# Kernel optimization log

Measured on AMD Instinct MI355X. Metric: run time of the kernel, lower is better.

Reference implementation:

```python
import jax, jax.numpy as jnp
import numpy as np
from jax import lax

HEADS = 16
HEAD_DIM = 64
EPS = 1e-5

def _act_quant(x):
    # per-token int8 absmax quantization (BitNet b1.58)
    scale = 127.0 / jnp.clip(jnp.max(jnp.abs(x), axis=-1, keepdims=True), EPS)
    return jnp.clip(jnp.round(x * scale), -128.0, 127.0) / scale

def _weight_quant(w):
    # ternary weight quantization with mean-absmax scale
    scale = 1.0 / jnp.clip(jnp.mean(jnp.abs(w)), EPS)
    return jnp.clip(jnp.round(w * scale), -1.0, 1.0) / scale

def bitlinear(x, w):
    # straight-through estimator: forward uses quantized, backward sees identity
    xq = x + lax.stop_gradient(_act_quant(x) - x)
    wq = w + lax.stop_gradient(_weight_quant(w) - w)
    return jnp.einsum('bsd,od->bso', xq, wq)

def setup_inputs() -> dict:
    key = jax.random.key(0)
    ks = jax.random.split(key, 5)
    B, S, D = 2, 2048, 1024
    x = jax.random.normal(ks[0], (B, S, D), dtype=jnp.float32)
    # causal mask (B, 1, S, S): 1 = keep, 0 = masked
    mask = jnp.broadcast_to(jnp.tril(jnp.ones((S, S), dtype=jnp.int32))[None, None], (B, 1, S, S))
    scale = 0.02
    Wq = jax.random.normal(ks[1], (D, D), dtype=jnp.float32) * scale
    Wk = jax.random.normal(ks[2], (D, D), dtype=jnp.float32) * scale
    Wv = jax.random.normal(ks[3], (D, D), dtype=jnp.float32) * scale
    Wo = jax.random.normal(ks[4], (D, D), dtype=jnp.float32) * scale
    return {"x": x, "mask": mask, "Wq": Wq, "Wk": Wk, "Wv": Wv, "Wo": Wo}

def reference(x, mask, Wq, Wk, Wv, Wo):
    B, S, D = x.shape
    H, Hd = HEADS, HEAD_DIM
    q = bitlinear(x, Wq).reshape(B, S, H, Hd).transpose(0, 2, 1, 3)  # (B,H,S,Hd)
    k = bitlinear(x, Wk).reshape(B, S, H, Hd).transpose(0, 2, 1, 3)
    v = bitlinear(x, Wv).reshape(B, S, H, Hd).transpose(0, 2, 1, 3)
    attn = jnp.einsum('bhsd,bhtd->bhst', q, k) / jnp.sqrt(jnp.float32(Hd))
    attn = jnp.where(mask == 0, -jnp.inf, attn)
    attn = jax.nn.softmax(attn, axis=-1)
    out = jnp.einsum('bhst,bhtd->bhsd', attn, v)
    out = out.transpose(0, 2, 1, 3).reshape(B, S, D)
    return bitlinear(out, Wo)
```

## Files before the change

### kernel.cpp

```cpp
#include <hip/hip_runtime.h>
#include <hip/hip_bf16.h>
#include <math.h>


typedef float  f32x4  __attribute__((ext_vector_type(4)));
typedef __bf16 bf16x8 __attribute__((ext_vector_type(8)));
typedef __bf16 bf16x4 __attribute__((ext_vector_type(4)));
typedef unsigned int u32x4 __attribute__((ext_vector_type(4)));

#define EPSV 1e-5f

__device__ __forceinline__ f32x4 mfma16(bf16x8 a, bf16x8 b, f32x4 c) {
    return __builtin_amdgcn_mfma_f32_16x16x32_bf16(a, b, c, 0, 0, 0);
}

__device__ __forceinline__ void gload16(const void* g, void* lds) {
    __builtin_amdgcn_global_load_lds((const __attribute__((address_space(1))) unsigned int*)g,
                                     (__attribute__((address_space(3))) unsigned int*)lds, 16, 0, 0);
}

__global__ __launch_bounds__(256) void k_wsum(const float* __restrict__ w0, const float* __restrict__ w1,
                                              const float* __restrict__ w2, const float* __restrict__ w3,
                                              double* __restrict__ wsum) {
    int w = blockIdx.x >> 6, chunk = blockIdx.x & 63, tid = threadIdx.x;
    const float* W = (w == 0) ? w0 : (w == 1) ? w1 : (w == 2) ? w2 : w3;
    const float* base = W + (size_t)chunk * 16384;
    float s = 0.f;
#pragma unroll
    for (int i = 0; i < 16; i++) {
        f32x4 v = *(const f32x4*)(base + i * 1024 + tid * 4);
        s += fabsf(v.x) + fabsf(v.y) + fabsf(v.z) + fabsf(v.w);
    }
#pragma unroll
    for (int off = 1; off < 64; off <<= 1) s += __shfl_xor(s, off);
    __shared__ float red[4];
    if ((tid & 63) == 0) red[tid >> 6] = s;
    __syncthreads();
    if (tid == 0) {
        double t = (double)red[0] + (double)red[1] + (double)red[2] + (double)red[3];
        atomicAdd(&wsum[w], t);
    }
}

__global__ __launch_bounds__(256) void k_wquant(const float* __restrict__ w0, const float* __restrict__ w1,
                                                const float* __restrict__ w2, const float* __restrict__ w3,
                                                const double* __restrict__ wsum,
                                                __bf16* __restrict__ wq, float* __restrict__ wm) {
    int w = blockIdx.y;
    const float* W = (w == 0) ? w0 : (w == 1) ? w1 : (w == 2) ? w2 : w3;
    float mean = (float)(wsum[w] * (1.0 / 1048576.0));
    float ms = fmaxf(mean, EPSV);
    float scale = 1.0f / ms;
    int pos = blockIdx.x * 1024 + threadIdx.x * 4;
    f32x4 v = *(const f32x4*)(W + pos);
    float q0 = fminf(fmaxf(rintf(v.x * scale), -1.f), 1.f);
    float q1 = fminf(fmaxf(rintf(v.y * scale), -1.f), 1.f);
    float q2 = fminf(fmaxf(rintf(v.z * scale), -1.f), 1.f);
    float q3 = fminf(fmaxf(rintf(v.w * scale), -1.f), 1.f);
    unsigned int b0 = __builtin_bit_cast(unsigned short, (__bf16)q0);
    unsigned int b1 = __builtin_bit_cast(unsigned short, (__bf16)q1);
    unsigned int b2 = __builtin_bit_cast(unsigned short, (__bf16)q2);
    unsigned int b3 = __builtin_bit_cast(unsigned short, (__bf16)q3);
    uint2 p; p.x = b0 | (b1 << 16); p.y = b2 | (b3 << 16);
    *(uint2*)(wq + (size_t)w * 1048576 + pos) = p;
    if (blockIdx.x == 0 && threadIdx.x == 0) wm[w] = ms;
}

__global__ __launch_bounds__(256) void k_actq(const float* __restrict__ in, __bf16* __restrict__ outq,
                                              float* __restrict__ rs) {
    int t = blockIdx.x, tid = threadIdx.x;
    const float* row = in + (size_t)t * 1024;
    f32x4 v = *(const f32x4*)(row + tid * 4);
    float am = fmaxf(fmaxf(fabsf(v.x), fabsf(v.y)), fmaxf(fabsf(v.z), fabsf(v.w)));
#pragma unroll
    for (int off = 1; off < 64; off <<= 1) am = fmaxf(am, __shfl_xor(am, off));
    __shared__ float red[4];
    if ((tid & 63) == 0) red[tid >> 6] = am;
    __syncthreads();
    am = fmaxf(fmaxf(red[0], red[1]), fmaxf(red[2], red[3]));
    am = fmaxf(am, EPSV);
    float scale = 127.0f / am;
    float q0 = fminf(fmaxf(rintf(v.x * scale), -128.f), 127.f);
    float q1 = fminf(fmaxf(rintf(v.y * scale), -128.f), 127.f);
    float q2 = fminf(fmaxf(rintf(v.z * scale), -128.f), 127.f);
    float q3 = fminf(fmaxf(rintf(v.w * scale), -128.f), 127.f);
    unsigned int b0 = __builtin_bit_cast(unsigned short, (__bf16)q0);
    unsigned int b1 = __builtin_bit_cast(unsigned short, (__bf16)q1);
    unsigned int b2 = __builtin_bit_cast(unsigned short, (__bf16)q2);
    unsigned int b3 = __builtin_bit_cast(unsigned short, (__bf16)q3);
    uint2 p; p.x = b0 | (b1 << 16); p.y = b2 | (b3 << 16);
    *(uint2*)(outq + (size_t)t * 1024 + tid * 4) = p;
    if (tid == 0) rs[t] = am / 127.0f;
}

template <int MODE>
__global__ __launch_bounds__(256) void k_gemm(const __bf16* __restrict__ X, const __bf16* __restrict__ Wb,
                                              const float* __restrict__ rs, const float* __restrict__ wm,
                                              __bf16* __restrict__ o0, __bf16* __restrict__ o1,
                                              __bf16* __restrict__ o2, float* __restrict__ outf) {
    __shared__ __attribute__((aligned(16))) __bf16 As[128 * 32];
    __shared__ __attribute__((aligned(16))) __bf16 Bs[128 * 32];
    int tid = threadIdx.x;
    int wave = tid >> 6, lane = tid & 63, g = lane >> 4, l = lane & 15;
    int m0 = blockIdx.x * 128, n0 = blockIdx.y * 128;
    int z = blockIdx.z;
    const __bf16* W = Wb + (size_t)z * 1048576;
    float wmv = wm[z];
    f32x4 acc[4][4] = {};
    int srow0 = wave * 16 + (lane >> 2);
    int scol = (lane & 3) * 8;
    const __bf16* Ag = X + (size_t)(m0 + srow0) * 1024 + scol;
    const __bf16* Bg = W + (size_t)(n0 + srow0) * 1024 + scol;
    __bf16* ldsA = As + wave * 512;
    __bf16* ldsB = Bs + wave * 512;
    int wrow = (wave >> 1) * 64, wcol = (wave & 1) * 64;
    bool vswap = (MODE == 0) && (z == 2);
    for (int k0 = 0; k0 < 1024; k0 += 32) {
        __syncthreads();
        gload16(Ag + k0,             ldsA);
        gload16(Ag + 64 * 1024 + k0, ldsA + 2048);
        gload16(Bg + k0,             ldsB);
        gload16(Bg + 64 * 1024 + k0, ldsB + 2048);
        __syncthreads();
        bf16x8 af[4], bfr[4];
#pragma unroll
        for (int i = 0; i < 4; i++) af[i]  = *(const bf16x8*)&As[(wrow + i * 16 + l) * 32 + 8 * g];
#pragma unroll
        for (int i = 0; i < 4; i++) bfr[i] = *(const bf16x8*)&Bs[(wcol + i * 16 + l) * 32 + 8 * g];
        if (vswap) {
#pragma unroll
            for (int mi = 0; mi < 4; mi++)
#pragma unroll
                for (int ni = 0; ni < 4; ni++)
                    acc[mi][ni] = mfma16(bfr[ni], af[mi], acc[mi][ni]);
        } else {
#pragma unroll
            for (int mi = 0; mi < 4; mi++)
#pragma unroll
                for (int ni = 0; ni < 4; ni++)
                    acc[mi][ni] = mfma16(af[mi], bfr[ni], acc[mi][ni]);
        }
    }
    if (vswap) {
#pragma unroll
        for (int mi = 0; mi < 4; mi++) {
            int m = m0 + wrow + mi * 16 + l;
            float rsm = rs[m] * wmv;
            int b = m >> 11, s2 = m & 2047;
#pragma unroll
            for (int ni = 0; ni < 4; ni++) {
                int nb = n0 + wcol + ni * 16 + 4 * g;
#pragma unroll
                for (int r = 0; r < 4; r++) {
                    int n = nb + r;
                    int h = n >> 6, hd = n & 63;
                    o2[((size_t)(b * 16 + h) * 64 + hd) * 2048 + s2] = (__bf16)(acc[mi][ni][r] * rsm);
                }
            }
        }
        return;
    }
#pragma unroll
    for (int mi = 0; mi < 4; mi++) {
        int mbase = m0 + wrow + mi * 16 + 4 * g;
        f32x4 rv = {rs[mbase], rs[mbase + 1], rs[mbase + 2], rs[mbase + 3]};
#pragma unroll
        for (int ni = 0; ni < 4; ni++) {
            int n = n0 + wcol + ni * 16 + l;
#pragma unroll
            for (int r = 0; r < 4; r++) {
                float v = acc[mi][ni][r] * (rv[r] * wmv);
                if constexpr (MODE == 0) {
                    int m = mbase + r;
                    int b = m >> 11, s2 = m & 2047;
                    int h = n >> 6, hd = n & 63;
                    __bf16* dst = (z == 0) ? o0 : o1;
                    dst[(((size_t)(b * 16 + h)) * 2048 + s2) * 64 + hd] = (__bf16)v;
                } else {
                    outf[(size_t)(mbase + r) * 1024 + n] = v;
                }
            }
        }
    }
}

__global__ __launch_bounds__(512) void k_attn(const __bf16* __restrict__ qg, const __bf16* __restrict__ kb,
                                              const __bf16* __restrict__ vt, float* __restrict__ attn) {
    __shared__ __attribute__((aligned(16))) __bf16 Ks[3][4096];
    __shared__ __attribute__((aligned(16))) __bf16 Vs[3][4096];
    int tid = threadIdx.x, w = tid >> 6, lane = tid & 63, g = lane >> 4, l = lane & 15;
    int bh = blockIdx.y, bq = bh >> 4, h = bh & 15;
    int q0 = blockIdx.x * 128;
    size_t bhq = (size_t)bh * 2048 * 64;
    int qlo = q0 + w * 16, qmax = qlo + 15;
    int qrow = qlo + l;
    bf16x8 aq0 = *(const bf16x8*)(qg + bhq + (size_t)qrow * 64 + 8 * g);
    bf16x8 aq1 = *(const bf16x8*)(qg + bhq + (size_t)qrow * 64 + 32 + 8 * g);
    asm volatile("" : "+v"(aq0), "+v"(aq1));
    f32x4 o[4] = {};
    float mreg = -INFINITY, lsum = 0.f;
    int sRow = w * 8 + (lane >> 3);
    int sCol = ((lane & 7) ^ (lane >> 3)) << 3;
    const __bf16* Kg = kb + bhq + (size_t)sRow * 64 + sCol;
    const __bf16* Vg = vt + bhq + (size_t)sRow * 2048 + sCol;
    int nt = 2 * (blockIdx.x + 1);
    gload16(Kg,        &Ks[0][w * 512]);
    gload16(Vg,        &Vs[0][w * 512]);
    gload16(Kg + 4096, &Ks[1][w * 512]);
    gload16(Vg + 64,   &Vs[1][w * 512]);
    int cur = 0;
    int swk = (l & 7) << 4;
    for (int t = 0; t < nt; ++t) {
        if (t < nt - 1) { asm volatile("s_waitcnt vmcnt(2)"); }
        else            { asm volatile("s_waitcnt vmcnt(0)"); }
        __builtin_amdgcn_s_barrier();
        __builtin_amdgcn_sched_barrier(0);
        int tn = t + 2;
        if (tn < nt) {
            int nbuf = cur + 2; if (nbuf >= 3) nbuf -= 3;
            gload16(Kg + (size_t)tn * 4096, &Ks[nbuf][w * 512]);
            gload16(Vg + tn * 64,           &Vs[nbuf][w * 512]);
        }
        int t0 = t * 64;
        if (t0 <= qmax) {
            const char* Kb = (const char*)&Ks[cur][0];
            const char* Vb = (const char*)&Vs[cur][0];
            f32x4 sv[4];
            __builtin_amdgcn_s_setprio(1);
#pragma unroll
            for (int nb = 0; nb < 4; nb++) {
                const char* kbase = Kb + (nb * 16 + l) * 128;
                bf16x8 bk0 = *(const bf16x8*)(kbase + ((16 * g) ^ swk));
                bf16x8 bk1 = *(const bf16x8*)(kbase + ((64 + 16 * g) ^ swk));
                f32x4 a = {};
                a = mfma16(bk0, aq0, a);
                a = mfma16(bk1, aq1, a);
                sv[nb] = a * 0.125f;
            }
            __builtin_amdgcn_s_setprio(0);
            if (t0 + 63 > qlo) {
#pragma unroll
                for (int nb = 0; nb < 4; nb++)
#pragma unroll
                    for (int r = 0; r < 4; r++) {
                        int key = t0 + nb * 16 + 4 * g + r;
                        if (key > qrow) sv[nb][r] = -INFINITY;
                    }
            }
            float pm0 = fmaxf(fmaxf(sv[0][0], sv[0][1]), fmaxf(sv[0][2], sv[0][3]));
            float pm1 = fmaxf(fmaxf(sv[1][0], sv[1][1]), fmaxf(sv[1][2], sv[1][3]));
            float pm2 = fmaxf(fmaxf(sv[2][0], sv[2][1]), fmaxf(sv[2][2], sv[2][3]));
            float pm3 = fmaxf(fmaxf(sv[3][0], sv[3][1]), fmaxf(sv[3][2], sv[3][3]));
            float pm = fmaxf(fmaxf(pm0, pm1), fmaxf(pm2, pm3));
            pm = fmaxf(pm, __shfl_xor(pm, 16));
            pm = fmaxf(pm, __shfl_xor(pm, 32));
            float mnew = fmaxf(mreg, pm);
            float corr = __expf(mreg - mnew);
            mreg = mnew;
            float psum = 0.f;
#pragma unroll
            for (int nb = 0; nb < 4; nb++)
#pragma unroll
                for (int r = 0; r < 4; r++) {
                    float pe = __expf(sv[nb][r] - mnew);
                    sv[nb][r] = pe;
                    psum += pe;
                }
            psum += __shfl_xor(psum, 16);
            psum += __shfl_xor(psum, 32);
            lsum = lsum * corr + psum;
#pragma unroll
            for (int hb = 0; hb < 4; hb++) o[hb] *= corr;
            bf16x8 pf0, pf1;
#pragma unroll
            for (int j = 0; j < 8; j++) {
                pf0[j] = (__bf16)sv[j >> 2][j & 3];
                pf1[j] = (__bf16)sv[2 + (j >> 2)][j & 3];
            }
            __builtin_amdgcn_s_setprio(1);
#pragma unroll
            for (int hb = 0; hb < 4; hb++) {
                int vrow = hb * 16 + l;
                const char* vb = Vb + vrow * 128;
                int rsw = vrow & 7;
                int ib = 8 * (g & 1);
                int gh = g >> 1;
                bf16x4 v00 = *(const bf16x4*)(vb + 16 * ((gh + 0) ^ rsw) + ib);
                bf16x4 v01 = *(const bf16x4*)(vb + 16 * ((gh + 2) ^ rsw) + ib);
                bf16x8 vf0 = __builtin_shufflevector(v00, v01, 0, 1, 2, 3, 4, 5, 6, 7);
                o[hb] = mfma16(vf0, pf0, o[hb]);
                bf16x4 v10 = *(const bf16x4*)(vb + 16 * ((gh + 4) ^ rsw) + ib);
                bf16x4 v11 = *(const bf16x4*)(vb + 16 * ((gh + 6) ^ rsw) + ib);
                bf16x8 vf1 = __builtin_shufflevector(v10, v11, 0, 1, 2, 3, 4, 5, 6, 7);
                o[hb] = mfma16(vf1, pf1, o[hb]);
            }
            __builtin_amdgcn_s_setprio(0);
        }
        cur = (cur + 1 == 3) ? 0 : cur + 1;
    }
    float inv = 1.0f / lsum;
    float* dst = attn + ((size_t)(bq * 2048 + qlo + l)) * 1024 + h * 64 + 4 * g;
#pragma unroll
    for (int hb = 0; hb < 4; hb++) {
        f32x4 vsto = o[hb] * inv;
        *(f32x4*)(dst + 16 * hb) = vsto;
    }
}

extern "C" void kernel_launch(void* const* d_in, const int* in_sizes, int n_in,
                              void* d_out, int out_size, void* d_ws, size_t ws_size,
                              hipStream_t stream) {
    const float* x  = (const float*)d_in[0];
    const float* Wq = (const float*)d_in[2];
    const float* Wk = (const float*)d_in[3];
    const float* Wv = (const float*)d_in[4];
    const float* Wo = (const float*)d_in[5];
    float* out = (float*)d_out;
    char* ws = (char*)d_ws;

    double* wsumd = (double*)(ws + 0);
    float*  wmv   = (float*)(ws + 256);
    __bf16* wqall = (__bf16*)(ws + 512);
    __bf16* xq    = (__bf16*)(ws + 512 + 8388608);
    float*  rsx   = (float*)(ws + 512 + 16777216);
    float*  rso   = (float*)(ws + 512 + 16777216 + 16384);
    char*   big   = ws + 512 + 16777216 + 32768;
    __bf16* qbuf  = (__bf16*)(big);
    __bf16* kbuf  = (__bf16*)(big + 8388608);
    __bf16* oq    = (__bf16*)(big + 16777216);
    __bf16* vtb   = (__bf16*)(big + 25165824);
    float*  attn  = (float*)(big + 33554432);

    hipMemsetAsync(ws, 0, 512, stream);
    k_wsum<<<dim3(256), 256, 0, stream>>>(Wq, Wk, Wv, Wo, wsumd);
    k_wquant<<<dim3(1024, 4), 256, 0, stream>>>(Wq, Wk, Wv, Wo, wsumd, wqall, wmv);
    k_actq<<<dim3(4096), 256, 0, stream>>>(x, xq, rsx);
    k_gemm<0><<<dim3(32, 8, 3), 256, 0, stream>>>(xq, wqall, rsx, wmv, qbuf, kbuf, vtb, nullptr);
    k_attn<<<dim3(16, 32), 512, 0, stream>>>(qbuf, kbuf, vtb, attn);
    k_actq<<<dim3(4096), 256, 0, stream>>>(attn, oq, rso);
    k_gemm<1><<<dim3(32, 8, 1), 256, 0, stream>>>(oq, wqall + 3 * 1048576, rso, wmv + 3,
                                                  nullptr, nullptr, nullptr, out);
}
```

Measured before the change: 254.1 us.

## Double-buffer GEMM LDS tiles and balance causal attention block scheduling

The GEMM kernel now uses two LDS buffers, prefetching the next K-slice while computing on the current one, with a single barrier per iteration instead of two. The attention kernel remaps query tile indices so blocks with long and short causal ranges are interleaved across the grid for better load balance. Drawbacks: LDS use doubles, and the barrier's implicit vmcnt wait may still serialise part of the prefetch.

```diff
diff --git a/kernel.cpp b/kernel.cpp
--- a/kernel.cpp
+++ b/kernel.cpp
@@ -98,8 +98,8 @@
                                               const float* __restrict__ rs, const float* __restrict__ wm,
                                               __bf16* __restrict__ o0, __bf16* __restrict__ o1,
                                               __bf16* __restrict__ o2, float* __restrict__ outf) {
-    __shared__ __attribute__((aligned(16))) __bf16 As[128 * 32];
-    __shared__ __attribute__((aligned(16))) __bf16 Bs[128 * 32];
+    __shared__ __attribute__((aligned(16))) __bf16 As[2][4096];
+    __shared__ __attribute__((aligned(16))) __bf16 Bs[2][4096];
     int tid = threadIdx.x;
     int wave = tid >> 6, lane = tid & 63, g = lane >> 4, l = lane & 15;
     int m0 = blockIdx.x * 128, n0 = blockIdx.y * 128;
@@ -111,22 +111,28 @@
     int scol = (lane & 3) * 8;
     const __bf16* Ag = X + (size_t)(m0 + srow0) * 1024 + scol;
     const __bf16* Bg = W + (size_t)(n0 + srow0) * 1024 + scol;
-    __bf16* ldsA = As + wave * 512;
-    __bf16* ldsB = Bs + wave * 512;
+    int woff = wave * 512;
     int wrow = (wave >> 1) * 64, wcol = (wave & 1) * 64;
     bool vswap = (MODE == 0) && (z == 2);
+    gload16(Ag,             &As[0][woff]);
+    gload16(Ag + 64 * 1024, &As[0][woff + 2048]);
+    gload16(Bg,             &Bs[0][woff]);
+    gload16(Bg + 64 * 1024, &Bs[0][woff + 2048]);
+    __syncthreads();
     for (int k0 = 0; k0 < 1024; k0 += 32) {
-        __syncthreads();
-        gload16(Ag + k0,             ldsA);
-        gload16(Ag + 64 * 1024 + k0, ldsA + 2048);
-        gload16(Bg + k0,             ldsB);
-        gload16(Bg + 64 * 1024 + k0, ldsB + 2048);
-        __syncthreads();
+        int cur = (k0 >> 5) & 1;
+        if (k0 + 32 < 1024) {
+            int nxt = cur ^ 1;
+            gload16(Ag + k0 + 32,             &As[nxt][woff]);
+            gload16(Ag + 64 * 1024 + k0 + 32, &As[nxt][woff + 2048]);
+            gload16(Bg + k0 + 32,             &Bs[nxt][woff]);
+            gload16(Bg + 64 * 1024 + k0 + 32, &Bs[nxt][woff + 2048]);
+        }
         bf16x8 af[4], bfr[4];
 #pragma unroll
-        for (int i = 0; i < 4; i++) af[i]  = *(const bf16x8*)&As[(wrow + i * 16 + l) * 32 + 8 * g];
-#pragma unroll
-        for (int i = 0; i < 4; i++) bfr[i] = *(const bf16x8*)&Bs[(wcol + i * 16 + l) * 32 + 8 * g];
+        for (int i = 0; i < 4; i++) af[i]  = *(const bf16x8*)&As[cur][(wrow + i * 16 + l) * 32 + 8 * g];
+#pragma unroll
+        for (int i = 0; i < 4; i++) bfr[i] = *(const bf16x8*)&Bs[cur][(wcol + i * 16 + l) * 32 + 8 * g];
         if (vswap) {
 #pragma unroll
             for (int mi = 0; mi < 4; mi++)
@@ -140,6 +146,7 @@
                 for (int ni = 0; ni < 4; ni++)
                     acc[mi][ni] = mfma16(af[mi], bfr[ni], acc[mi][ni]);
         }
+        __syncthreads();
     }
     if (vswap) {
 #pragma unroll
@@ -190,7 +197,9 @@
     __shared__ __attribute__((aligned(16))) __bf16 Vs[3][4096];
     int tid = threadIdx.x, w = tid >> 6, lane = tid & 63, g = lane >> 4, l = lane & 15;
     int bh = blockIdx.y, bq = bh >> 4, h = bh & 15;
-    int q0 = blockIdx.x * 128;
+    int xt = (blockIdx.x + blockIdx.y) & 15;
+    int xs = (blockIdx.y & 16) ? (15 - xt) : xt;
+    int q0 = xs * 128;
     size_t bhq = (size_t)bh * 2048 * 64;
     int qlo = q0 + w * 16, qmax = qlo + 15;
     int qrow = qlo + l;
@@ -203,7 +212,7 @@
     int sCol = ((lane & 7) ^ (lane >> 3)) << 3;
     const __bf16* Kg = kb + bhq + (size_t)sRow * 64 + sCol;
     const __bf16* Vg = vt + bhq + (size_t)sRow * 2048 + sCol;
-    int nt = 2 * (blockIdx.x + 1);
+    int nt = 2 * (xs + 1);
     gload16(Kg,        &Ks[0][w * 512]);
     gload16(Vg,        &Vs[0][w * 512]);
     gload16(Kg + 4096, &Ks[1][w * 512]);
```

Result: faster. 242.9 us (-4.4%).

## Double-buffer GEMM LDS tiles with swizzle and rebalance causal attention block order

Applied to the files above, without the earlier changes.

The GEMM moves from a single-buffered 32-wide K tile to a double-buffered 64-wide K tile. It uses an XOR-swizzled LDS layout and raises wave priority around the MFMA bursts, so global-to-LDS loads overlap compute, there are fewer barriers, and bank conflicts drop. The attention kernel remaps block indices so heavy and light causal query tiles interleave in launch order, which should give better load balance across CUs. In exchange, the GEMM uses more LDS, which may lower occupancy, and the index math gets more complex.

```diff
diff --git a/kernel.cpp b/kernel.cpp
--- a/kernel.cpp
+++ b/kernel.cpp
@@ -98,8 +98,8 @@
                                               const float* __restrict__ rs, const float* __restrict__ wm,
                                               __bf16* __restrict__ o0, __bf16* __restrict__ o1,
                                               __bf16* __restrict__ o2, float* __restrict__ outf) {
-    __shared__ __attribute__((aligned(16))) __bf16 As[128 * 32];
-    __shared__ __attribute__((aligned(16))) __bf16 Bs[128 * 32];
+    __shared__ __attribute__((aligned(16))) __bf16 As[2][8192];
+    __shared__ __attribute__((aligned(16))) __bf16 Bs[2][8192];
     int tid = threadIdx.x;
     int wave = tid >> 6, lane = tid & 63, g = lane >> 4, l = lane & 15;
     int m0 = blockIdx.x * 128, n0 = blockIdx.y * 128;
@@ -107,39 +107,60 @@
     const __bf16* W = Wb + (size_t)z * 1048576;
     float wmv = wm[z];
     f32x4 acc[4][4] = {};
-    int srow0 = wave * 16 + (lane >> 2);
-    int scol = (lane & 3) * 8;
-    const __bf16* Ag = X + (size_t)(m0 + srow0) * 1024 + scol;
-    const __bf16* Bg = W + (size_t)(n0 + srow0) * 1024 + scol;
-    __bf16* ldsA = As + wave * 512;
-    __bf16* ldsB = Bs + wave * 512;
+    int sRow = wave * 32 + (lane >> 3);
+    int sCol = 8 * ((lane & 7) ^ (lane >> 3));
+    const __bf16* Ag = X + (size_t)(m0 + sRow) * 1024 + sCol;
+    const __bf16* Bg = W + (size_t)(n0 + sRow) * 1024 + sCol;
     int wrow = (wave >> 1) * 64, wcol = (wave & 1) * 64;
     bool vswap = (MODE == 0) && (z == 2);
-    for (int k0 = 0; k0 < 1024; k0 += 32) {
+#pragma unroll
+    for (int j = 0; j < 4; j++) {
+        gload16(Ag + (size_t)j * 8192, &As[0][(wave * 4 + j) * 512]);
+        gload16(Bg + (size_t)j * 8192, &Bs[0][(wave * 4 + j) * 512]);
+    }
+    __syncthreads();
+    for (int t = 0; t < 16; ++t) {
+        int cur = t & 1;
+        if (t < 15) {
+            int nxt = cur ^ 1;
+            int ko = (t + 1) * 64;
+#pragma unroll
+            for (int j = 0; j < 4; j++) {
+                gload16(Ag + (size_t)j * 8192 + ko, &As[nxt][(wave * 4 + j) * 512]);
+                gload16(Bg + (size_t)j * 8192 + ko, &Bs[nxt][(wave * 4 + j) * 512]);
+            }
+        }
+        bf16x8 af[4][2], bfr[4][2];
+        int c0 = 8 * ((0 * 4 + g) ^ (l & 7));
+        int c1 = 8 * ((1 * 4 + g) ^ (l & 7));
+#pragma unroll
+        for (int i = 0; i < 4; i++) {
+            const __bf16* ra = &As[cur][(wrow + i * 16 + l) * 64];
+            const __bf16* rb = &Bs[cur][(wcol + i * 16 + l) * 64];
+            af[i][0]  = *(const bf16x8*)(ra + c0);
+            af[i][1]  = *(const bf16x8*)(ra + c1);
+            bfr[i][0] = *(const bf16x8*)(rb + c0);
+            bfr[i][1] = *(const bf16x8*)(rb + c1);
+        }
+        __builtin_amdgcn_s_setprio(1);
+#pragma unroll
+        for (int ks = 0; ks < 2; ks++) {
+            if (vswap) {
+#pragma unroll
+                for (int mi = 0; mi < 4; mi++)
+#pragma unroll
+                    for (int ni = 0; ni < 4; ni++)
+                        acc[mi][ni] = mfma16(bfr[ni][ks], af[mi][ks], acc[mi][ni]);
+            } else {
+#pragma unroll
+                for (int mi = 0; mi < 4; mi++)
+#pragma unroll
+                    for (int ni = 0; ni < 4; ni++)
+                        acc[mi][ni] = mfma16(af[mi][ks], bfr[ni][ks], acc[mi][ni]);
+            }
+        }
+        __builtin_amdgcn_s_setprio(0);
         __syncthreads();
-        gload16(Ag + k0,             ldsA);
-        gload16(Ag + 64 * 1024 + k0, ldsA + 2048);
-        gload16(Bg + k0,             ldsB);
-        gload16(Bg + 64 * 1024 + k0, ldsB + 2048);
-        __syncthreads();
-        bf16x8 af[4], bfr[4];
-#pragma unroll
-        for (int i = 0; i < 4; i++) af[i]  = *(const bf16x8*)&As[(wrow + i * 16 + l) * 32 + 8 * g];
-#pragma unroll
-        for (int i = 0; i < 4; i++) bfr[i] = *(const bf16x8*)&Bs[(wcol + i * 16 + l) * 32 + 8 * g];
-        if (vswap) {
-#pragma unroll
-            for (int mi = 0; mi < 4; mi++)
-#pragma unroll
-                for (int ni = 0; ni < 4; ni++)
-                    acc[mi][ni] = mfma16(bfr[ni], af[mi], acc[mi][ni]);
-        } else {
-#pragma unroll
-            for (int mi = 0; mi < 4; mi++)
-#pragma unroll
-                for (int ni = 0; ni < 4; ni++)
-                    acc[mi][ni] = mfma16(af[mi], bfr[ni], acc[mi][ni]);
-        }
     }
     if (vswap) {
 #pragma unroll
@@ -189,8 +210,13 @@
     __shared__ __attribute__((aligned(16))) __bf16 Ks[3][4096];
     __shared__ __attribute__((aligned(16))) __bf16 Vs[3][4096];
     int tid = threadIdx.x, w = tid >> 6, lane = tid & 63, g = lane >> 4, l = lane & 15;
-    int bh = blockIdx.y, bq = bh >> 4, h = bh & 15;
-    int q0 = blockIdx.x * 128;
+    int bx = blockIdx.x, by = blockIdx.y;
+    int bh = (bx & 7) | ((by & 3) << 3);
+    int u = bx >> 3, v = by >> 2;
+    int base2 = 2 * ((u << 2) | (v & 3));
+    int xs = (v < 4) ? base2 : 15 - base2;
+    int bq = bh >> 4, h = bh & 15;
+    int q0 = xs * 128;
     size_t bhq = (size_t)bh * 2048 * 64;
     int qlo = q0 + w * 16, qmax = qlo + 15;
     int qrow = qlo + l;
@@ -203,7 +229,7 @@
     int sCol = ((lane & 7) ^ (lane >> 3)) << 3;
     const __bf16* Kg = kb + bhq + (size_t)sRow * 64 + sCol;
     const __bf16* Vg = vt + bhq + (size_t)sRow * 2048 + sCol;
-    int nt = 2 * (blockIdx.x + 1);
+    int nt = 2 * (xs + 1);
     gload16(Kg,        &Ks[0][w * 512]);
     gload16(Vg,        &Vs[0][w * 512]);
     gload16(Kg + 4096, &Ks[1][w * 512]);
```

Result: faster. 229.1 us (-9.8%).
